# Optimization experiments

Hardware: AMD Instinct MI355X
Metric: run time of the kernel (lower is better)

The kernel has to match this reference:

```python
import jax, jax.numpy as jnp
import numpy as np

NEG_INF = -1e6  # matches d2l masked_softmax fill value


def masked_softmax(scores, valid_len):
    # scores: [B, Q, K]; valid_len: [B] int — keys at positions >= valid_len[b] are masked
    K = scores.shape[-1]
    mask = jnp.arange(K, dtype=jnp.int32)[None, None, :] < valid_len[:, None, None]
    scores = jnp.where(mask, scores, NEG_INF)
    return jax.nn.softmax(scores, axis=-1)


def setup_inputs() -> dict:
    key = jax.random.key(0)
    k1, k2, k3, k4 = jax.random.split(key, 4)
    B, S, D = 8, 4096, 64
    query = jax.random.normal(k1, (B, S, D), dtype=jnp.float32)
    key_t = jax.random.normal(k2, (B, S, D), dtype=jnp.float32)
    value = jax.random.normal(k3, (B, S, D), dtype=jnp.float32)
    valid_len = jax.random.randint(k4, (B,), 1, S + 1, dtype=jnp.int32)
    return {"query": query, "key": key_t, "value": value, "valid_len": valid_len}


def reference(query, key, value, valid_len):
    d = query.shape[-1]
    # [B, Q, K] score matrix (the module materializes it explicitly)
    scores = jnp.einsum("bqd,bkd->bqk", query, key) / jnp.sqrt(jnp.float32(d))
    attn = masked_softmax(scores, valid_len)
    # dropout p=0.0 (eval): identity
    out = jnp.einsum("bqk,bkd->bqd", attn, value)
    return out
```

## Files before the change

kernel.cpp:

```cpp
#include <hip/hip_runtime.h>
#include <stdint.h>


constexpr int BB = 8;
constexpr int SS = 4096;
constexpr int DH = 64;
constexpr int CH = 32;
constexpr int NKT = SS / CH;
constexpr int TILE_SHORTS = 8192;

typedef short  bfrag  __attribute__((ext_vector_type(8)));
typedef float  f32x16 __attribute__((ext_vector_type(16)));
typedef unsigned int uvec4 __attribute__((ext_vector_type(4)));

__device__ __forceinline__ unsigned short f2bf(float x) {
  unsigned u = __builtin_bit_cast(unsigned, x);
  u += 0x7fffu + ((u >> 16) & 1u);
  return (unsigned short)(u >> 16);
}
__device__ __forceinline__ float bf2f(unsigned short h) {
  return __builtin_bit_cast(float, ((unsigned)h) << 16);
}

__global__ __launch_bounds__(256) void prepack(
    const float* __restrict__ K, const float* __restrict__ V,
    short* __restrict__ ws) {
  const int b  = blockIdx.x >> 7;
  const int kt = blockIdx.x & 127;
  const int t  = threadIdx.x;
  short* tile = ws + (size_t)(b * NKT + kt) * TILE_SHORTS;

  {
    const int d8 = t >> 5, key = t & 31;
    const float* src = K + ((size_t)b * SS + kt * CH + key) * DH + d8 * 8;
    float4 a = ((const float4*)src)[0];
    float4 c = ((const float4*)src)[1];
    float v[8] = {a.x, a.y, a.z, a.w, c.x, c.y, c.z, c.w};
    bfrag hi, lo;
#pragma unroll
    for (int j = 0; j < 8; ++j) {
      unsigned short h = f2bf(v[j]);
      hi[j] = (short)h;
      lo[j] = (short)f2bf(v[j] - bf2f(h));
    }
    *(bfrag*)(tile + t * 8)        = hi;
    *(bfrag*)(tile + 2048 + t * 8) = lo;
  }
  {
    const int k8 = t >> 6, d = t & 63;
    const float* src = V + ((size_t)b * SS + kt * CH + k8 * 8) * DH + d;
    bfrag hi, lo;
#pragma unroll
    for (int j = 0; j < 8; ++j) {
      float x = src[j * DH];
      unsigned short h = f2bf(x);
      hi[j] = (short)h;
      lo[j] = (short)f2bf(x - bf2f(h));
    }
    *(bfrag*)(tile + 4096 + t * 8) = hi;
    *(bfrag*)(tile + 6144 + t * 8) = lo;
  }
}

__global__ __launch_bounds__(256) void attn_mfma(
    const float* __restrict__ Q, const short* __restrict__ wsT,
    const int* __restrict__ VL, float* __restrict__ Out) {
  __shared__ __align__(16) short sKV[2][2][TILE_SHORTS];

  const int tid = threadIdx.x;
  const int w   = tid >> 6;
  const int l   = tid & 63;
  const int rg  = w & 1;
  const int p   = w >> 1;
  const int hi5 = l >> 5;
  const int l31 = l & 31;
  const int b   = blockIdx.x & 7;
  const int qt  = blockIdx.x >> 3;
  const int vlen = VL[b];
  const int nch  = (vlen + CH - 1) / CH;

  bfrag qh[4], ql[4];
  {
    const float* qsrc = Q + ((size_t)b * SS + qt * 64 + rg * 32 + l31) * DH;
#pragma unroll
    for (int dt = 0; dt < 4; ++dt) {
      const float* pp = qsrc + dt * 16 + hi5 * 8;
      float4 a = ((const float4*)pp)[0];
      float4 c = ((const float4*)pp)[1];
      float v[8] = {a.x, a.y, a.z, a.w, c.x, c.y, c.z, c.w};
#pragma unroll
      for (int j = 0; j < 8; ++j) {
        float x = v[j] * 0.125f;
        unsigned short h = f2bf(x);
        qh[dt][j] = (short)h;
        ql[dt][j] = (short)f2bf(x - bf2f(h));
      }
    }
  }

  f32x16 o0, o1;
#pragma unroll
  for (int r = 0; r < 16; ++r) { o0[r] = 0.f; o1[r] = 0.f; }
  float m = -1e30f, lsum = 0.f;

  const short* tbase = wsT + (size_t)b * NKT * TILE_SHORTS;

  auto stage = [&](int ci, int buf) {
    const short* g = tbase + (size_t)ci * TILE_SHORTS + l * 8;
    short* dst = &sKV[p][buf][0];
#pragma unroll
    for (int j = 0; j < 8; ++j) {
      const int s = j * 2 + rg;
      __builtin_amdgcn_global_load_lds(
          (const __attribute__((address_space(1))) void*)(g + s * 512),
          (__attribute__((address_space(3))) void*)(dst + s * 512),
          16, 0, 0);
    }
  };

  if (p < nch) stage(p, 0);

  const int T = (nch + 1) >> 1;
  for (int t = 0; t < T; ++t) {
    __syncthreads();
    const int ci  = 2 * t + p;
    const int cur = t & 1;
    if (ci + 2 < nch) stage(ci + 2, cur ^ 1);
    if (ci < nch) {
      const short* t0 = &sKV[p][cur][0];

      f32x16 accA, accB;
#pragma unroll
      for (int r = 0; r < 16; ++r) { accA[r] = 0.f; accB[r] = 0.f; }
#pragma unroll
      for (int dt = 0; dt < 4; ++dt) {
        bfrag kh = *(const bfrag*)(t0 + ((2 * dt + hi5) * 32 + l31) * 8);
        bfrag kl = *(const bfrag*)(t0 + 2048 + ((2 * dt + hi5) * 32 + l31) * 8);
        accA = __builtin_amdgcn_mfma_f32_32x32x16_bf16(kh, qh[dt], accA, 0, 0, 0);
        if (dt < 2)
          accA = __builtin_amdgcn_mfma_f32_32x32x16_bf16(kh, ql[dt], accA, 0, 0, 0);
        else
          accB = __builtin_amdgcn_mfma_f32_32x32x16_bf16(kh, ql[dt], accB, 0, 0, 0);
        accB = __builtin_amdgcn_mfma_f32_32x32x16_bf16(kl, qh[dt], accB, 0, 0, 0);
      }
      float s[16];
#pragma unroll
      for (int r = 0; r < 16; ++r) s[r] = accA[r] + accB[r];

      const int c0 = ci * CH;
      if (c0 + CH > vlen) {
#pragma unroll
        for (int r = 0; r < 16; ++r) {
          int key = c0 + (r & 3) + 8 * (r >> 2) + 4 * hi5;
          if (key >= vlen) s[r] = -1e30f;
        }
      }

      float cmax = s[0];
#pragma unroll
      for (int r = 1; r < 16; ++r) cmax = fmaxf(cmax, s[r]);
      cmax = fmaxf(cmax, __shfl_xor(cmax, 32));

      if (__any((int)(cmax > m + 8.0f))) {
        float mn = fmaxf(m, cmax);
        float sc = __expf(m - mn);
        m = mn;
        lsum *= sc;
#pragma unroll
        for (int r = 0; r < 16; ++r) {
          float s2 = __shfl(sc, (r & 3) + 8 * (r >> 2) + 4 * hi5);
          o0[r] *= s2;
          o1[r] *= s2;
        }
      }

      float ps = 0.f;
#pragma unroll
      for (int r = 0; r < 16; ++r) {
        s[r] = __expf(s[r] - m);
        ps += s[r];
      }
      ps += __shfl_xor(ps, 32);
      lsum += ps;

      unsigned wh[8], wl[8];
#pragma unroll
      for (int i = 0; i < 8; ++i) {
        float p0 = s[2 * i], p1 = s[2 * i + 1];
        unsigned hw;
        asm("v_cvt_pk_bf16_f32 %0, %1, %2" : "=v"(hw) : "v"(p0), "v"(p1));
        float h0 = __builtin_bit_cast(float, hw << 16);
        float h1 = __builtin_bit_cast(float, hw & 0xffff0000u);
        float r0 = p0 - h0, r1 = p1 - h1;
        unsigned lw;
        asm("v_cvt_pk_bf16_f32 %0, %1, %2" : "=v"(lw) : "v"(r0), "v"(r1));
        wh[i] = hw;
        wl[i] = lw;
      }
      asm("v_permlane32_swap_b32 %0, %1" : "+v"(wh[0]), "+v"(wh[2]));
      asm("v_permlane32_swap_b32 %0, %1" : "+v"(wh[1]), "+v"(wh[3]));
      asm("v_permlane32_swap_b32 %0, %1" : "+v"(wh[4]), "+v"(wh[6]));
      asm("v_permlane32_swap_b32 %0, %1" : "+v"(wh[5]), "+v"(wh[7]));
      asm("v_permlane32_swap_b32 %0, %1" : "+v"(wl[0]), "+v"(wl[2]));
      asm("v_permlane32_swap_b32 %0, %1" : "+v"(wl[1]), "+v"(wl[3]));
      asm("v_permlane32_swap_b32 %0, %1" : "+v"(wl[4]), "+v"(wl[6]));
      asm("v_permlane32_swap_b32 %0, %1" : "+v"(wl[5]), "+v"(wl[7]));
      bfrag ph[2], pl[2];
      {
        uvec4 u0 = {wh[0], wh[1], wh[2], wh[3]};
        uvec4 u1 = {wh[4], wh[5], wh[6], wh[7]};
        uvec4 u2 = {wl[0], wl[1], wl[2], wl[3]};
        uvec4 u3 = {wl[4], wl[5], wl[6], wl[7]};
        ph[0] = __builtin_bit_cast(bfrag, u0);
        ph[1] = __builtin_bit_cast(bfrag, u1);
        pl[0] = __builtin_bit_cast(bfrag, u2);
        pl[1] = __builtin_bit_cast(bfrag, u3);
      }

#pragma unroll
      for (int ks = 0; ks < 2; ++ks) {
        const int vo = ((2 * ks + hi5) * 64 + l31) * 8;
        bfrag vh0 = *(const bfrag*)(t0 + 4096 + vo);
        bfrag vl0 = *(const bfrag*)(t0 + 6144 + vo);
        bfrag vh1 = *(const bfrag*)(t0 + 4096 + vo + 256);
        bfrag vl1 = *(const bfrag*)(t0 + 6144 + vo + 256);
        o0 = __builtin_amdgcn_mfma_f32_32x32x16_bf16(ph[ks], vh0, o0, 0, 0, 0);
        o0 = __builtin_amdgcn_mfma_f32_32x32x16_bf16(ph[ks], vl0, o0, 0, 0, 0);
        o0 = __builtin_amdgcn_mfma_f32_32x32x16_bf16(pl[ks], vh0, o0, 0, 0, 0);
        o1 = __builtin_amdgcn_mfma_f32_32x32x16_bf16(ph[ks], vh1, o1, 0, 0, 0);
        o1 = __builtin_amdgcn_mfma_f32_32x32x16_bf16(ph[ks], vl1, o1, 0, 0, 0);
        o1 = __builtin_amdgcn_mfma_f32_32x32x16_bf16(pl[ks], vh1, o1, 0, 0, 0);
      }
    }
  }

  float* fl = (float*)&sKV[0][0][0];
  __syncthreads();
  if (hi5 == 0) {
    fl[p * 64 + rg * 32 + l31]       = m;
    fl[128 + p * 64 + rg * 32 + l31] = lsum;
  }
  __syncthreads();
  const float mo = fl[(p ^ 1) * 64 + rg * 32 + l31];
  const float lo = fl[128 + (p ^ 1) * 64 + rg * 32 + l31];
  const float M  = fmaxf(m, mo);
  const float wgt = __expf(m - M);
  const float Lsum = lsum * wgt + lo * __expf(mo - M);
  const float linv = 1.0f / Lsum;
  float* C = fl + 256 + rg * 2048;
  if (p == 1) {
#pragma unroll
    for (int r = 0; r < 16; ++r) {
      int row = (r & 3) + 8 * (r >> 2) + 4 * hi5;
      float wr = __shfl(wgt, row);
      C[row * 64 + l31]      = wr * o0[r];
      C[row * 64 + 32 + l31] = wr * o1[r];
    }
  }
  __syncthreads();
  if (p == 0) {
    float* ob = Out + ((size_t)b * SS + qt * 64 + rg * 32) * DH;
#pragma unroll
    for (int r = 0; r < 16; ++r) {
      int row = (r & 3) + 8 * (r >> 2) + 4 * hi5;
      float wr = __shfl(wgt, row);
      float li = __shfl(linv, row);
      ob[row * DH + l31]      = (wr * o0[r] + C[row * 64 + l31]) * li;
      ob[row * DH + 32 + l31] = (wr * o1[r] + C[row * 64 + 32 + l31]) * li;
    }
  }
}

__global__ __launch_bounds__(256) void attn_naive(
    const float* __restrict__ Q, const float* __restrict__ K,
    const float* __restrict__ V, const int* __restrict__ VL,
    float* __restrict__ Out) {
  const int row = blockIdx.x * 256 + threadIdx.x;
  const int b = row >> 12;
  const int vlen = VL[b];
  const float* q = Q + (size_t)row * DH;
  float qr[DH];
#pragma unroll
  for (int d = 0; d < DH; ++d) qr[d] = q[d] * 0.125f;
  float m = -1e30f, ls = 0.f, o[DH];
#pragma unroll
  for (int d = 0; d < DH; ++d) o[d] = 0.f;
  const float* Kb = K + (size_t)b * SS * DH;
  const float* Vb = V + (size_t)b * SS * DH;
  for (int k = 0; k < vlen; ++k) {
    float sc = 0.f;
    for (int d = 0; d < DH; ++d) sc += qr[d] * Kb[(size_t)k * DH + d];
    if (sc > m) {
      float scale = __expf(m - sc);
      m = sc;
      ls *= scale;
      for (int d = 0; d < DH; ++d) o[d] *= scale;
    }
    float pv = __expf(sc - m);
    ls += pv;
    for (int d = 0; d < DH; ++d) o[d] += pv * Vb[(size_t)k * DH + d];
  }
  for (int d = 0; d < DH; ++d) Out[(size_t)row * DH + d] = o[d] / ls;
}

extern "C" void kernel_launch(void* const* d_in, const int* in_sizes, int n_in,
                              void* d_out, int out_size, void* d_ws,
                              size_t ws_size, hipStream_t stream) {
  const float* Q  = (const float*)d_in[0];
  const float* K  = (const float*)d_in[1];
  const float* V  = (const float*)d_in[2];
  const int*   VL = (const int*)d_in[3];
  float* Out = (float*)d_out;

  const size_t need = (size_t)BB * NKT * TILE_SHORTS * sizeof(short);
  if (ws_size >= need) {
    prepack<<<dim3(BB * NKT), dim3(256), 0, stream>>>(K, V, (short*)d_ws);
    attn_mfma<<<dim3(BB * (SS / 64)), dim3(256), 0, stream>>>(
        Q, (const short*)d_ws, VL, Out);
  } else {
    attn_naive<<<dim3(BB * SS / 256), dim3(256), 0, stream>>>(Q, K, V, VL, Out);
  }
}
```

Measured before the change: 179.6 us.

## Split KV sequence across blocks with combine kernel; load V directly from global

```diff
diff --git a/kernel.cpp b/kernel.cpp
--- a/kernel.cpp
+++ b/kernel.cpp
@@ -8,6 +8,7 @@
 constexpr int CH = 32;
 constexpr int NKT = SS / CH;
 constexpr int TILE_SHORTS = 8192;
+constexpr int KO_SHORTS = 4096;
 
 typedef short  bfrag  __attribute__((ext_vector_type(8)));
 typedef float  f32x16 __attribute__((ext_vector_type(16)));
@@ -62,11 +63,17 @@
   }
 }
 
-__global__ __launch_bounds__(256) void attn_mfma(
+__global__ __launch_bounds__(256, 4) void attn_mfma(
     const float* __restrict__ Q, const short* __restrict__ wsT,
-    const int* __restrict__ VL, float* __restrict__ Out) {
-  __shared__ __align__(16) short sKV[2][2][TILE_SHORTS];
-
+    const int* __restrict__ VL, float* __restrict__ Out,
+    float* __restrict__ part_o, float* __restrict__ part_ml,
+    int nsl, int sc) {
+  __shared__ __align__(16) short sKV[2][2][KO_SHORTS];
+
+  const int blk = blockIdx.x;
+  const int slice = blk >> 9;
+  const int b   = (blk + slice) & 7;
+  const int qt  = (blk >> 3) & 63;
   const int tid = threadIdx.x;
   const int w   = tid >> 6;
   const int l   = tid & 63;
@@ -74,10 +81,15 @@
   const int p   = w >> 1;
   const int hi5 = l >> 5;
   const int l31 = l & 31;
-  const int b   = blockIdx.x & 7;
-  const int qt  = blockIdx.x >> 3;
+
   const int vlen = VL[b];
   const int nch  = (vlen + CH - 1) / CH;
+  int nact = (nch + sc - 1) / sc;
+  if (nact > nsl) nact = nsl;
+  if (slice >= nact) return;
+  const int c_lo = slice * sc;
+  const int c_hi = min(c_lo + sc, nch);
+  const int nchS = c_hi - c_lo;
 
   bfrag qh[4], ql[4];
   {
@@ -106,27 +118,27 @@
   const short* tbase = wsT + (size_t)b * NKT * TILE_SHORTS;
 
   auto stage = [&](int ci, int buf) {
-    const short* g = tbase + (size_t)ci * TILE_SHORTS + l * 8;
+    const short* g = tbase + (size_t)ci * TILE_SHORTS;
     short* dst = &sKV[p][buf][0];
 #pragma unroll
-    for (int j = 0; j < 8; ++j) {
+    for (int j = 0; j < 4; ++j) {
       const int s = j * 2 + rg;
       __builtin_amdgcn_global_load_lds(
-          (const __attribute__((address_space(1))) void*)(g + s * 512),
-          (__attribute__((address_space(3))) void*)(dst + s * 512),
+          (const __attribute__((address_space(1))) void*)(g + s * 512 + l * 8),
+          (__attribute__((address_space(3))) void*)(dst + s * 512 + l * 8),
           16, 0, 0);
     }
   };
 
-  if (p < nch) stage(p, 0);
-
-  const int T = (nch + 1) >> 1;
+  if (c_lo + p < c_hi) stage(c_lo + p, 0);
+
+  const int T = (nchS + 1) >> 1;
   for (int t = 0; t < T; ++t) {
     __syncthreads();
-    const int ci  = 2 * t + p;
+    const int ci  = c_lo + 2 * t + p;
     const int cur = t & 1;
-    if (ci + 2 < nch) stage(ci + 2, cur ^ 1);
-    if (ci < nch) {
+    if (ci + 2 < c_hi) stage(ci + 2, cur ^ 1);
+    if (ci < c_hi) {
       const short* t0 = &sKV[p][cur][0];
 
       f32x16 accA, accB;
@@ -143,9 +155,21 @@
           accB = __builtin_amdgcn_mfma_f32_32x32x16_bf16(kh, ql[dt], accB, 0, 0, 0);
         accB = __builtin_amdgcn_mfma_f32_32x32x16_bf16(kl, qh[dt], accB, 0, 0, 0);
       }
+
       float s[16];
 #pragma unroll
       for (int r = 0; r < 16; ++r) s[r] = accA[r] + accB[r];
+
+      const short* gV = tbase + (size_t)ci * TILE_SHORTS;
+      bfrag vh[2][2], vl[2][2];
+#pragma unroll
+      for (int ks = 0; ks < 2; ++ks) {
+        const int vo = ((2 * ks + hi5) * 64 + l31) * 8;
+        vh[ks][0] = *(const bfrag*)(gV + 4096 + vo);
+        vl[ks][0] = *(const bfrag*)(gV + 6144 + vo);
+        vh[ks][1] = *(const bfrag*)(gV + 4096 + vo + 256);
+        vl[ks][1] = *(const bfrag*)(gV + 6144 + vo + 256);
+      }
 
       const int c0 = ci * CH;
       if (c0 + CH > vlen) {
@@ -163,12 +187,12 @@
 
       if (__any((int)(cmax > m + 8.0f))) {
         float mn = fmaxf(m, cmax);
-        float sc = __expf(m - mn);
+        float sc2 = __expf(m - mn);
         m = mn;
-        lsum *= sc;
+        lsum *= sc2;
 #pragma unroll
         for (int r = 0; r < 16; ++r) {
-          float s2 = __shfl(sc, (r & 3) + 8 * (r >> 2) + 4 * hi5);
+          float s2 = __shfl(sc2, (r & 3) + 8 * (r >> 2) + 4 * hi5);
           o0[r] *= s2;
           o1[r] *= s2;
         }
@@ -183,7 +207,7 @@
       ps += __shfl_xor(ps, 32);
       lsum += ps;
 
-      unsigned wh[8], wl[8];
+      unsigned wh[8], wl2[8];
 #pragma unroll
       for (int i = 0; i < 8; ++i) {
         float p0 = s[2 * i], p1 = s[2 * i + 1];
@@ -195,22 +219,22 @@
         unsigned lw;
         asm("v_cvt_pk_bf16_f32 %0, %1, %2" : "=v"(lw) : "v"(r0), "v"(r1));
         wh[i] = hw;
-        wl[i] = lw;
+        wl2[i] = lw;
       }
       asm("v_permlane32_swap_b32 %0, %1" : "+v"(wh[0]), "+v"(wh[2]));
       asm("v_permlane32_swap_b32 %0, %1" : "+v"(wh[1]), "+v"(wh[3]));
       asm("v_permlane32_swap_b32 %0, %1" : "+v"(wh[4]), "+v"(wh[6]));
       asm("v_permlane32_swap_b32 %0, %1" : "+v"(wh[5]), "+v"(wh[7]));
-      asm("v_permlane32_swap_b32 %0, %1" : "+v"(wl[0]), "+v"(wl[2]));
-      asm("v_permlane32_swap_b32 %0, %1" : "+v"(wl[1]), "+v"(wl[3]));
-      asm("v_permlane32_swap_b32 %0, %1" : "+v"(wl[4]), "+v"(wl[6]));
-      asm("v_permlane32_swap_b32 %0, %1" : "+v"(wl[5]), "+v"(wl[7]));
+      asm("v_permlane32_swap_b32 %0, %1" : "+v"(wl2[0]), "+v"(wl2[2]));
+      asm("v_permlane32_swap_b32 %0, %1" : "+v"(wl2[1]), "+v"(wl2[3]));
+      asm("v_permlane32_swap_b32 %0, %1" : "+v"(wl2[4]), "+v"(wl2[6]));
+      asm("v_permlane32_swap_b32 %0, %1" : "+v"(wl2[5]), "+v"(wl2[7]));
       bfrag ph[2], pl[2];
       {
         uvec4 u0 = {wh[0], wh[1], wh[2], wh[3]};
         uvec4 u1 = {wh[4], wh[5], wh[6], wh[7]};
-        uvec4 u2 = {wl[0], wl[1], wl[2], wl[3]};
-        uvec4 u3 = {wl[4], wl[5], wl[6], wl[7]};
+        uvec4 u2 = {wl2[0], wl2[1], wl2[2], wl2[3]};
+        uvec4 u3 = {wl2[4], wl2[5], wl2[6], wl2[7]};
         ph[0] = __builtin_bit_cast(bfrag, u0);
         ph[1] = __builtin_bit_cast(bfrag, u1);
         pl[0] = __builtin_bit_cast(bfrag, u2);
@@ -219,17 +243,12 @@
 
 #pragma unroll
       for (int ks = 0; ks < 2; ++ks) {
-        const int vo = ((2 * ks + hi5) * 64 + l31) * 8;
-        bfrag vh0 = *(const bfrag*)(t0 + 4096 + vo);
-        bfrag vl0 = *(const bfrag*)(t0 + 6144 + vo);
-        bfrag vh1 = *(const bfrag*)(t0 + 4096 + vo + 256);
-        bfrag vl1 = *(const bfrag*)(t0 + 6144 + vo + 256);
-        o0 = __builtin_amdgcn_mfma_f32_32x32x16_bf16(ph[ks], vh0, o0, 0, 0, 0);
-        o0 = __builtin_amdgcn_mfma_f32_32x32x16_bf16(ph[ks], vl0, o0, 0, 0, 0);
-        o0 = __builtin_amdgcn_mfma_f32_32x32x16_bf16(pl[ks], vh0, o0, 0, 0, 0);
-        o1 = __builtin_amdgcn_mfma_f32_32x32x16_bf16(ph[ks], vh1, o1, 0, 0, 0);
-        o1 = __builtin_amdgcn_mfma_f32_32x32x16_bf16(ph[ks], vl1, o1, 0, 0, 0);
-        o1 = __builtin_amdgcn_mfma_f32_32x32x16_bf16(pl[ks], vh1, o1, 0, 0, 0);
+        o0 = __builtin_amdgcn_mfma_f32_32x32x16_bf16(ph[ks], vh[ks][0], o0, 0, 0, 0);
+        o0 = __builtin_amdgcn_mfma_f32_32x32x16_bf16(ph[ks], vl[ks][0], o0, 0, 0, 0);
+        o0 = __builtin_amdgcn_mfma_f32_32x32x16_bf16(pl[ks], vh[ks][0], o0, 0, 0, 0);
+        o1 = __builtin_amdgcn_mfma_f32_32x32x16_bf16(ph[ks], vh[ks][1], o1, 0, 0, 0);
+        o1 = __builtin_amdgcn_mfma_f32_32x32x16_bf16(ph[ks], vl[ks][1], o1, 0, 0, 0);
+        o1 = __builtin_amdgcn_mfma_f32_32x32x16_bf16(pl[ks], vh[ks][1], o1, 0, 0, 0);
       }
     }
   }
@@ -241,11 +260,11 @@
     fl[128 + p * 64 + rg * 32 + l31] = lsum;
   }
   __syncthreads();
-  const float mo = fl[(p ^ 1) * 64 + rg * 32 + l31];
-  const float lo = fl[128 + (p ^ 1) * 64 + rg * 32 + l31];
-  const float M  = fmaxf(m, mo);
+  const float mo  = fl[(p ^ 1) * 64 + rg * 32 + l31];
+  const float lo_ = fl[128 + (p ^ 1) * 64 + rg * 32 + l31];
+  const float M   = fmaxf(m, mo);
   const float wgt = __expf(m - M);
-  const float Lsum = lsum * wgt + lo * __expf(mo - M);
+  const float Lsum = lsum * wgt + lo_ * __expf(mo - M);
   const float linv = 1.0f / Lsum;
   float* C = fl + 256 + rg * 2048;
   if (p == 1) {
@@ -259,15 +278,88 @@
   }
   __syncthreads();
   if (p == 0) {
-    float* ob = Out + ((size_t)b * SS + qt * 64 + rg * 32) * DH;
-#pragma unroll
-    for (int r = 0; r < 16; ++r) {
-      int row = (r & 3) + 8 * (r >> 2) + 4 * hi5;
-      float wr = __shfl(wgt, row);
-      float li = __shfl(linv, row);
-      ob[row * DH + l31]      = (wr * o0[r] + C[row * 64 + l31]) * li;
-      ob[row * DH + 32 + l31] = (wr * o1[r] + C[row * 64 + 32 + l31]) * li;
-    }
+    if (nact == 1) {
+      float* ob = Out + ((size_t)b * SS + qt * 64 + rg * 32) * DH;
+#pragma unroll
+      for (int r = 0; r < 16; ++r) {
+        int row = (r & 3) + 8 * (r >> 2) + 4 * hi5;
+        float wr = __shfl(wgt, row);
+        float li = __shfl(linv, row);
+        ob[row * DH + l31]      = (wr * o0[r] + C[row * 64 + l31]) * li;
+        ob[row * DH + 32 + l31] = (wr * o1[r] + C[row * 64 + 32 + l31]) * li;
+      }
+    } else {
+      const size_t base = (size_t)(b * 64 + qt) * nsl + slice;
+      float* po = part_o + base * 4096 + rg * 32 * 64;
+#pragma unroll
+      for (int r = 0; r < 16; ++r) {
+        int row = (r & 3) + 8 * (r >> 2) + 4 * hi5;
+        float wr = __shfl(wgt, row);
+        po[row * 64 + l31]      = wr * o0[r] + C[row * 64 + l31];
+        po[row * 64 + 32 + l31] = wr * o1[r] + C[row * 64 + 32 + l31];
+      }
+      if (hi5 == 0) {
+        part_ml[base * 128 + (rg * 32 + l31) * 2 + 0] = M;
+        part_ml[base * 128 + (rg * 32 + l31) * 2 + 1] = Lsum;
+      }
+    }
+  }
+}
+
+__global__ __launch_bounds__(256) void combine(
+    const float* __restrict__ part_o, const float* __restrict__ part_ml,
+    const int* __restrict__ VL, float* __restrict__ Out, int nsl, int sc) {
+  const int blk = blockIdx.x;
+  const int b = blk & 7, qt = blk >> 3;
+  const int vlen = VL[b];
+  const int nch = (vlen + CH - 1) / CH;
+  int nact = (nch + sc - 1) / sc;
+  if (nact > nsl) nact = nsl;
+  if (nact < 2) return;
+  const int row = threadIdx.x >> 2;
+  const int seg = (threadIdx.x & 3) * 16;
+  const size_t base = (size_t)(b * 64 + qt) * nsl;
+
+  float ms[4], ls[4];
+  float M = -1e30f;
+#pragma unroll
+  for (int s = 0; s < 4; ++s) {
+    if (s < nact) {
+      ms[s] = part_ml[(base + s) * 128 + row * 2 + 0];
+      ls[s] = part_ml[(base + s) * 128 + row * 2 + 1];
+      M = fmaxf(M, ms[s]);
+    } else { ms[s] = -1e30f; ls[s] = 0.f; }
+  }
+  float L = 0.f;
+#pragma unroll
+  for (int s = 0; s < 4; ++s) {
+    ms[s] = __expf(ms[s] - M);
+    L += ms[s] * ls[s];
+  }
+  const float linv = 1.0f / L;
+  float4 acc[4];
+#pragma unroll
+  for (int j = 0; j < 4; ++j) acc[j] = make_float4(0.f, 0.f, 0.f, 0.f);
+#pragma unroll
+  for (int s = 0; s < 4; ++s) {
+    if (s < nact) {
+      const float4* po =
+          (const float4*)(part_o + (base + s) * 4096 + row * 64 + seg);
+#pragma unroll
+      for (int j = 0; j < 4; ++j) {
+        float4 v = po[j];
+        acc[j].x += ms[s] * v.x;
+        acc[j].y += ms[s] * v.y;
+        acc[j].z += ms[s] * v.z;
+        acc[j].w += ms[s] * v.w;
+      }
+    }
+  }
+  float4* op = (float4*)(Out + ((size_t)b * SS + qt * 64 + row) * DH + seg);
+#pragma unroll
+  for (int j = 0; j < 4; ++j) {
+    acc[j].x *= linv; acc[j].y *= linv; acc[j].z *= linv; acc[j].w *= linv;
+    op[j] = acc[j];
   }
 }
 
@@ -312,11 +404,24 @@
   const int*   VL = (const int*)d_in[3];
   float* Out = (float*)d_out;
 
-  const size_t need = (size_t)BB * NKT * TILE_SHORTS * sizeof(short);
-  if (ws_size >= need) {
-    prepack<<<dim3(BB * NKT), dim3(256), 0, stream>>>(K, V, (short*)d_ws);
-    attn_mfma<<<dim3(BB * (SS / 64)), dim3(256), 0, stream>>>(
-        Q, (const short*)d_ws, VL, Out);
+  const size_t pack_bytes = (size_t)BB * NKT * TILE_SHORTS * sizeof(short);
+  const size_t po_bytes   = (size_t)512 * 4 * 4096 * sizeof(float);
+  const size_t pml_bytes  = (size_t)512 * 4 * 128 * sizeof(float);
+  const size_t need_split = pack_bytes + po_bytes + pml_bytes;
+
+  if (ws_size >= need_split) {
+    short* pack = (short*)d_ws;
+    float* po   = (float*)((char*)d_ws + pack_bytes);
+    float* pml  = (float*)((char*)d_ws + pack_bytes + po_bytes);
+    prepack<<<dim3(BB * NKT), dim3(256), 0, stream>>>(K, V, pack);
+    attn_mfma<<<dim3(4 * 512), dim3(256), 0, stream>>>(
+        Q, pack, VL, Out, po, pml, 4, 32);
+    combine<<<dim3(512), dim3(256), 0, stream>>>(po, pml, VL, Out, 4, 32);
+  } else if (ws_size >= pack_bytes) {
+    short* pack = (short*)d_ws;
+    prepack<<<dim3(BB * NKT), dim3(256), 0, stream>>>(K, V, pack);
+    attn_mfma<<<dim3(512), dim3(256), 0, stream>>>(
+        Q, pack, VL, Out, (float*)d_ws, (float*)d_ws, 1, NKT);
   } else {
     attn_naive<<<dim3(BB * SS / 256), dim3(256), 0, stream>>>(Q, K, V, VL, Out);
   }
```

Result: slower. 218.1 us (+21.5%).
